# Kernel tuning notes

Measured on AMD Instinct MI355X. Metric: run time of the kernel, lower is better.

The kernel has to match this reference:

```python
import jax, jax.numpy as jnp
import numpy as np

NUM_HEADS = 8


def setup_inputs() -> dict:
    key = jax.random.key(0)
    k1, k2, k3, k4 = jax.random.split(key, 4)
    E = 256
    seq = jax.random.normal(k1, (4, 256, E, 16, 16), dtype=jnp.float32)
    W_qkv = jax.random.normal(k2, (3 * E, E), dtype=jnp.float32) * (E ** -0.5)
    W_out = jax.random.normal(k3, (E, E), dtype=jnp.float32) * (E ** -0.5)
    b_out = jax.random.normal(k4, (E,), dtype=jnp.float32)
    return {"seq": seq, "W_qkv": W_qkv, "W_out": W_out, "b_out": b_out,
            "n_sub_x": 16, "n_sub_y": 16}


def reference(seq, W_qkv, W_out, b_out, n_sub_x, n_sub_y):
    # seq: [b, s, c, h, w] -- a sequence of functions (tokens on spatial grids)
    b, s, c, h, w = seq.shape
    H = NUM_HEADS
    d = c // H  # head_dim

    # pointwise QKV projection along the channel axis (no bias)
    qkv = jnp.einsum('oc,bscxy->bsoxy', W_qkv, seq)  # [b, s, 3c, h, w]
    # channel layout per einops: (num_heads, split=3, head_dim)
    qkv = qkv.reshape(b, s, H, 3, d, h, w)
    qkv = jnp.transpose(qkv, (3, 0, 2, 1, 4, 5, 6))  # [3, b, H, s, d, h, w]
    q, k, v = qkv[0], qkv[1], qkv[2]

    # func_attention: L2 inner product over head_dim and spatial dims
    scale = 1.0 / np.sqrt(d * h * w).astype(np.float32)
    scores = jnp.einsum('bhqdxy,bhkdxy->bhqk', q, k) * scale  # [b, H, s, s]
    attn = jax.nn.softmax(scores, axis=-1)
    sa = jnp.einsum('bhqk,bhkdxy->bhqdxy', attn, v)  # [b, H, s, d, h, w]

    # merge heads back to channel axis: 'b h s d ... -> b s (h d) ...'
    sa = jnp.transpose(sa, (0, 2, 1, 3, 4, 5)).reshape(b, s, c, h, w)

    # output projection (with bias) along channels
    out = jnp.einsum('oc,bscxy->bsoxy', W_out, sa)
    out = out + b_out[None, None, :, None, None]
    return out
```

## Files before the change

kernel.cpp:

```cpp
#include <hip/hip_runtime.h>
#include <stdint.h>


#define DI __device__ __forceinline__

typedef __attribute__((ext_vector_type(4))) float  f32x4;
typedef __attribute__((ext_vector_type(8))) short  s16x8;
typedef __attribute__((ext_vector_type(4))) short  s16x4;
typedef __attribute__((ext_vector_type(8))) __bf16 bf16x8;

DI unsigned short f2bf(float f) {
    unsigned int u = __builtin_bit_cast(unsigned int, f);
    u = (u + 0x7fffu + ((u >> 16) & 1u)) >> 16;
    return (unsigned short)u;
}
DI bf16x8 asbf(s16x8 v) { return __builtin_bit_cast(bf16x8, v); }
#define MFMA16(a, b, c) __builtin_amdgcn_mfma_f32_16x16x32_bf16((a), (b), (c), 0, 0, 0)

DI void stage_a256(unsigned short* __restrict__ T,
                   const unsigned short* __restrict__ src, int stride, int tid) {
    const unsigned short* s = src + (size_t)tid * stride;
    int r7 = tid & 7;
#pragma unroll
    for (int ch = 0; ch < 8; ch++) {
        s16x8 v = *(const s16x8*)(s + ch * 8);
        *(s16x8*)&T[tid * 64 + ((ch ^ r7) << 3)] = v;
    }
}

DI void stage_l128(unsigned short* __restrict__ T,
                   const unsigned short* __restrict__ src, int stride, int tid) {
    int row = tid >> 1, c4 = (tid & 1) * 4, r7 = row & 7;
    const unsigned short* s = src + (size_t)row * stride;
#pragma unroll
    for (int i = 0; i < 4; i++) {
        s16x8 v = *(const s16x8*)(s + (c4 + i) * 8);
        *(s16x8*)&T[row * 64 + (((c4 + i) ^ r7) << 3)] = v;
    }
}

DI void stage_tr16(unsigned short* __restrict__ BT,
                   const unsigned short* __restrict__ src, int stride, int tid) {
    int p = tid & 127, cqh = tid >> 7, p7 = p & 7;
#pragma unroll
    for (int i = 0; i < 8; i++) {
        int cq = cqh + 2 * i;
        int cb = cq * 4;
        unsigned short e0 = src[(size_t)(cb + 0) * stride + p];
        unsigned short e1 = src[(size_t)(cb + 1) * stride + p];
        unsigned short e2 = src[(size_t)(cb + 2) * stride + p];
        unsigned short e3 = src[(size_t)(cb + 3) * stride + p];
        s16x4 v = {(short)e0, (short)e1, (short)e2, (short)e3};
        *(s16x4*)&BT[p * 64 + (((cq >> 1) ^ p7) << 3) + (cq & 1) * 4] = v;
    }
}

DI void stage_tr32(unsigned short* __restrict__ BT,
                   const float* __restrict__ src, int stride, int tid) {
    int p = tid & 127, cqh = tid >> 7, p7 = p & 7;
#pragma unroll
    for (int i = 0; i < 8; i++) {
        int cq = cqh + 2 * i;
        int cb = cq * 4;
        float e0 = src[(size_t)(cb + 0) * stride + p];
        float e1 = src[(size_t)(cb + 1) * stride + p];
        float e2 = src[(size_t)(cb + 2) * stride + p];
        float e3 = src[(size_t)(cb + 3) * stride + p];
        s16x4 v = {(short)f2bf(e0), (short)f2bf(e1), (short)f2bf(e2), (short)f2bf(e3)};
        *(s16x4*)&BT[p * 64 + (((cq >> 1) ^ p7) << 3) + (cq & 1) * 4] = v;
    }
}

DI void mfma_84(const unsigned short* __restrict__ Al,
                const unsigned short* __restrict__ Bl,
                f32x4 acc[8][4], int wm, int wn, int lg, int lr) {
#pragma unroll
    for (int kk = 0; kk < 2; kk++) {
        int off = (((kk * 4 + lg) ^ (lr & 7)) << 3);
        s16x8 af[8];
#pragma unroll
        for (int m = 0; m < 8; m++)
            af[m] = *(const s16x8*)&Al[(wm + m * 16 + lr) * 64 + off];
        s16x8 bf[4];
#pragma unroll
        for (int n = 0; n < 4; n++)
            bf[n] = *(const s16x8*)&Bl[(wn + n * 16 + lr) * 64 + off];
#pragma unroll
        for (int n = 0; n < 4; n++) {
            bf16x8 bv = asbf(bf[n]);
#pragma unroll
            for (int m = 0; m < 8; m++)
                acc[m][n] = MFMA16(asbf(af[m]), bv, acc[m][n]);
        }
    }
}

DI void mfma_44(const unsigned short* __restrict__ Al,
                const unsigned short* __restrict__ Bl,
                f32x4 acc[4][4], int wm, int wn, int lg, int lr) {
#pragma unroll
    for (int kk = 0; kk < 2; kk++) {
        int off = (((kk * 4 + lg) ^ (lr & 7)) << 3);
        s16x8 af[4];
#pragma unroll
        for (int m = 0; m < 4; m++)
            af[m] = *(const s16x8*)&Al[(wm + m * 16 + lr) * 64 + off];
        s16x8 bf[4];
#pragma unroll
        for (int n = 0; n < 4; n++)
            bf[n] = *(const s16x8*)&Bl[(wn + n * 16 + lr) * 64 + off];
#pragma unroll
        for (int n = 0; n < 4; n++) {
            bf16x8 bv = asbf(bf[n]);
#pragma unroll
            for (int m = 0; m < 4; m++)
                acc[m][n] = MFMA16(asbf(af[m]), bv, acc[m][n]);
        }
    }
}

__global__ __launch_bounds__(64) void k_prep(
    const float* __restrict__ Wqkv, const float* __restrict__ Wout,
    unsigned short* __restrict__ Wbf)
{
    int r = blockIdx.x, ln = threadIdx.x;
    const float* src;
    if (r < 768) {
        int split = r >> 8, hd = r & 255;
        src = Wqkv + (size_t)(((hd >> 5) * 96) + split * 32 + (hd & 31)) * 256;
    } else {
        src = Wout + (size_t)(r - 768) * 256;
    }
    f32x4 v = *(const f32x4*)(src + ln * 4);
    s16x4 h = {(short)f2bf(v.x), (short)f2bf(v.y), (short)f2bf(v.z), (short)f2bf(v.w)};
    *(s16x4*)&Wbf[(size_t)r * 256 + ln * 4] = h;
}

__global__ __launch_bounds__(256, 2) void k_qkv(
    const float* __restrict__ seq, const unsigned short* __restrict__ Wbf,
    unsigned short* __restrict__ Qb, unsigned short* __restrict__ Kb,
    unsigned short* __restrict__ Vb)
{
    const int bid = blockIdx.x;
    const int wk = (bid & 7) * 768 + (bid >> 3);
    const int bs = wk / 6, r6 = wk - bs * 6;
    const int mt = r6 >> 1, nt = r6 & 1;
    const int b = bs >> 8, s = bs & 255;
    const int tid = threadIdx.x, ln = tid & 63, wv = tid >> 6;
    const int wm = (wv >> 1) * 128, wn = (wv & 1) * 64;
    const int lg = ln >> 4, lr = ln & 15;

    __shared__ __align__(16) unsigned short Al[256 * 64];
    __shared__ __align__(16) unsigned short Bt[128 * 64];

    f32x4 acc[8][4];
    const f32x4 z4 = {0.f, 0.f, 0.f, 0.f};
#pragma unroll
    for (int m = 0; m < 8; m++)
#pragma unroll
        for (int n = 0; n < 4; n++) acc[m][n] = z4;

    const unsigned short* Asrc = Wbf + (size_t)mt * 256 * 256;
    const float* Bsrc = seq + (size_t)bs * 65536 + nt * 128;

    for (int k0 = 0; k0 < 256; k0 += 64) {
        stage_a256(Al, Asrc + k0, 256, tid);
        stage_tr32(Bt, Bsrc + (size_t)k0 * 256, 256, tid);
        __syncthreads();
        mfma_84(Al, Bt, acc, wm, wn, lg, lr);
        __syncthreads();
    }

    unsigned short* dst = (mt == 0) ? Qb : (mt == 1) ? Kb : Vb;
#pragma unroll
    for (int m = 0; m < 8; m++) {
#pragma unroll
        for (int rr = 0; rr < 4; rr++) {
            int o = wm + m * 16 + lg * 4 + rr;
            size_t base = ((size_t)((b * 8 + (o >> 5)) * 256 + s)) * 8192
                        + (size_t)(o & 31) * 256 + nt * 128 + wn + lr;
#pragma unroll
            for (int n = 0; n < 4; n++)
                dst[base + n * 16] = f2bf(acc[m][n][rr]);
        }
    }
}

__global__ __launch_bounds__(256, 3) void k_scores(
    const unsigned short* __restrict__ Qb, const unsigned short* __restrict__ Kb,
    float* __restrict__ Sp)
{
    const int bh = blockIdx.y;
    const int qt = blockIdx.x >> 2, kc = (blockIdx.x >> 1) & 1, st = blockIdx.x & 1;
    const int tid = threadIdx.x, ln = tid & 63, wv = tid >> 6;
    const int wm = (wv >> 1) * 64, wn = (wv & 1) * 64;
    const int lg = ln >> 4, lr = ln & 15;

    __shared__ __align__(16) unsigned short Al[128 * 64];
    __shared__ __align__(16) unsigned short Bl[128 * 64];

    f32x4 acc[4][4];
    const f32x4 z4 = {0.f, 0.f, 0.f, 0.f};
#pragma unroll
    for (int m = 0; m < 4; m++)
#pragma unroll
        for (int n = 0; n < 4; n++) acc[m][n] = z4;

    const unsigned short* Asrc = Qb + (size_t)(bh * 256 + qt * 128) * 8192 + kc * 4096;
    const unsigned short* Bsrc = Kb + (size_t)(bh * 256 + st * 128) * 8192 + kc * 4096;

    for (int t = 0; t < 64; t++) {
        stage_l128(Al, Asrc + t * 64, 8192, tid);
        stage_l128(Bl, Bsrc + t * 64, 8192, tid);
        __syncthreads();
        mfma_44(Al, Bl, acc, wm, wn, lg, lr);
        __syncthreads();
    }

    float* dst = Sp + (size_t)kc * 2097152
               + ((size_t)(bh * 256) + qt * 128 + wm) * 256 + st * 128 + wn;
#pragma unroll
    for (int m = 0; m < 4; m++) {
#pragma unroll
        for (int rr = 0; rr < 4; rr++) {
            float* d = dst + (size_t)(m * 16 + lg * 4 + rr) * 256 + lr;
#pragma unroll
            for (int n = 0; n < 4; n++)
                d[n * 16] = acc[m][n][rr];
        }
    }
}

__global__ __launch_bounds__(256) void k_softmax(
    const float* __restrict__ Sp, unsigned short* __restrict__ Pb)
{
    const int tid = threadIdx.x, ln = tid & 63;
    const int row = blockIdx.x * 4 + (tid >> 6);
    const float scale = 0.011048543456039806f;

    const float* p0 = Sp + (size_t)row * 256 + ln * 4;
    f32x4 a = *(const f32x4*)p0;
    f32x4 c = *(const f32x4*)(p0 + 2097152);
    f32x4 v = (a + c) * scale;

    float m = fmaxf(fmaxf(v.x, v.y), fmaxf(v.z, v.w));
#pragma unroll
    for (int off = 32; off; off >>= 1) m = fmaxf(m, __shfl_xor(m, off));
    float e0 = __expf(v.x - m), e1 = __expf(v.y - m);
    float e2 = __expf(v.z - m), e3 = __expf(v.w - m);
    float sum = e0 + e1 + e2 + e3;
#pragma unroll
    for (int off = 32; off; off >>= 1) sum += __shfl_xor(sum, off);
    float inv = 1.f / sum;
    s16x4 p = {(short)f2bf(e0 * inv), (short)f2bf(e1 * inv),
               (short)f2bf(e2 * inv), (short)f2bf(e3 * inv)};
    *(s16x4*)(Pb + (size_t)row * 256 + ln * 4) = p;
}

__global__ __launch_bounds__(256, 2) void k_av(
    const unsigned short* __restrict__ Pb, const unsigned short* __restrict__ Vb,
    unsigned short* __restrict__ SAb)
{
    const int ft = blockIdx.x, bh = blockIdx.y;
    const int b = bh >> 3, h = bh & 7;
    const int tid = threadIdx.x, ln = tid & 63, wv = tid >> 6;
    const int wm = (wv >> 1) * 128, wn = (wv & 1) * 64;
    const int lg = ln >> 4, lr = ln & 15;

    __shared__ __align__(16) unsigned short Al[256 * 64];
    __shared__ __align__(16) unsigned short Bt[128 * 64];

    f32x4 acc[8][4];
    const f32x4 z4 = {0.f, 0.f, 0.f, 0.f};
#pragma unroll
    for (int m = 0; m < 8; m++)
#pragma unroll
        for (int n = 0; n < 4; n++) acc[m][n] = z4;

    const unsigned short* Asrc = Pb + (size_t)(bh * 256) * 256;
    const unsigned short* Bsrc = Vb + (size_t)(bh * 256) * 8192 + ft * 128;

    for (int k0 = 0; k0 < 256; k0 += 64) {
        stage_a256(Al, Asrc + k0, 256, tid);
        stage_tr16(Bt, Bsrc + (size_t)k0 * 8192, 8192, tid);
        __syncthreads();
        mfma_84(Al, Bt, acc, wm, wn, lg, lr);
        __syncthreads();
    }

    const int cc = h * 32 + (ft >> 1);
    const int pb = (ft & 1) * 128;
#pragma unroll
    for (int m = 0; m < 8; m++) {
#pragma unroll
        for (int rr = 0; rr < 4; rr++) {
            int q = wm + m * 16 + lg * 4 + rr;
            size_t base = ((size_t)(b * 256 + q) * 256 + cc) * 256 + pb + wn + lr;
#pragma unroll
            for (int n = 0; n < 4; n++)
                SAb[base + n * 16] = f2bf(acc[m][n][rr]);
        }
    }
}

__global__ __launch_bounds__(256, 2) void k_out(
    const unsigned short* __restrict__ SAb, const unsigned short* __restrict__ Wbf,
    const float* __restrict__ bias, float* __restrict__ out)
{
    const int nt = blockIdx.x, bs = blockIdx.y;
    const int tid = threadIdx.x, ln = tid & 63, wv = tid >> 6;
    const int wm = (wv >> 1) * 128, wn = (wv & 1) * 64;
    const int lg = ln >> 4, lr = ln & 15;

    __shared__ __align__(16) unsigned short Al[256 * 64];
    __shared__ __align__(16) unsigned short Bt[128 * 64];

    f32x4 acc[8][4];
    const f32x4 z4 = {0.f, 0.f, 0.f, 0.f};
#pragma unroll
    for (int m = 0; m < 8; m++)
#pragma unroll
        for (int n = 0; n < 4; n++) acc[m][n] = z4;

    const unsigned short* Asrc = Wbf + (size_t)768 * 256;
    const unsigned short* Bsrc = SAb + (size_t)bs * 65536 + nt * 128;

    for (int k0 = 0; k0 < 256; k0 += 64) {
        stage_a256(Al, Asrc + k0, 256, tid);
        stage_tr16(Bt, Bsrc + (size_t)k0 * 256, 256, tid);
        __syncthreads();
        mfma_84(Al, Bt, acc, wm, wn, lg, lr);
        __syncthreads();
    }

#pragma unroll
    for (int m = 0; m < 8; m++) {
#pragma unroll
        for (int rr = 0; rr < 4; rr++) {
            int o = wm + m * 16 + lg * 4 + rr;
            float bo = bias[o];
            float* d = out + ((size_t)bs * 256 + o) * 256 + nt * 128 + wn + lr;
#pragma unroll
            for (int n = 0; n < 4; n++)
                d[n * 16] = acc[m][n][rr] + bo;
        }
    }
}

extern "C" void kernel_launch(void* const* d_in, const int* in_sizes, int n_in,
                              void* d_out, int out_size, void* d_ws, size_t ws_size,
                              hipStream_t stream)
{
    const float* seq  = (const float*)d_in[0];
    const float* Wqkv = (const float*)d_in[1];
    const float* Wout = (const float*)d_in[2];
    const float* bout = (const float*)d_in[3];

    unsigned short* Qb = (unsigned short*)d_out;
    unsigned short* Kb = Qb + 67108864;

    unsigned short* Vb  = (unsigned short*)d_ws;
    unsigned short* SAb = Vb + 67108864;
    float*          Sp  = (float*)SAb;
    unsigned short* Pb  = (unsigned short*)d_ws + 134217728;
    unsigned short* Wbf = Pb + 2097152;

    float* out = (float*)d_out;

    k_prep<<<dim3(1024), dim3(64), 0, stream>>>(Wqkv, Wout, Wbf);
    k_qkv<<<dim3(6144), dim3(256), 0, stream>>>(seq, Wbf, Qb, Kb, Vb);
    k_scores<<<dim3(8, 32), dim3(256), 0, stream>>>(Qb, Kb, Sp);
    k_softmax<<<dim3(2048), dim3(256), 0, stream>>>(Sp, Pb);
    k_av<<<dim3(64, 32), dim3(256), 0, stream>>>(Pb, Vb, SAb);
    k_out<<<dim3(2, 1024), dim3(256), 0, stream>>>(SAb, Wbf, bout, out);
}
```

Baseline: 604.8 us.

## Pre-transpose seq to bf16, split V projection with transposed layout, widen score split-K

```diff
diff --git a/kernel.cpp b/kernel.cpp
--- a/kernel.cpp
+++ b/kernel.cpp
@@ -39,34 +39,23 @@
     }
 }
 
-DI void stage_tr16(unsigned short* __restrict__ BT,
-                   const unsigned short* __restrict__ src, int stride, int tid) {
+DI void stage_tr16s(unsigned short* __restrict__ BT,
+                    const unsigned short* __restrict__ src, int stride, int tid) {
     int p = tid & 127, cqh = tid >> 7, p7 = p & 7;
+    unsigned short e[32];
+#pragma unroll
+    for (int i = 0; i < 8; i++) {
+        int cb = (cqh + 2 * i) * 4;
+        e[i * 4 + 0] = src[(size_t)(cb + 0) * stride + p];
+        e[i * 4 + 1] = src[(size_t)(cb + 1) * stride + p];
+        e[i * 4 + 2] = src[(size_t)(cb + 2) * stride + p];
+        e[i * 4 + 3] = src[(size_t)(cb + 3) * stride + p];
+    }
 #pragma unroll
     for (int i = 0; i < 8; i++) {
         int cq = cqh + 2 * i;
-        int cb = cq * 4;
-        unsigned short e0 = src[(size_t)(cb + 0) * stride + p];
-        unsigned short e1 = src[(size_t)(cb + 1) * stride + p];
-        unsigned short e2 = src[(size_t)(cb + 2) * stride + p];
-        unsigned short e3 = src[(size_t)(cb + 3) * stride + p];
-        s16x4 v = {(short)e0, (short)e1, (short)e2, (short)e3};
-        *(s16x4*)&BT[p * 64 + (((cq >> 1) ^ p7) << 3) + (cq & 1) * 4] = v;
-    }
-}
-
-DI void stage_tr32(unsigned short* __restrict__ BT,
-                   const float* __restrict__ src, int stride, int tid) {
-    int p = tid & 127, cqh = tid >> 7, p7 = p & 7;
-#pragma unroll
-    for (int i = 0; i < 8; i++) {
-        int cq = cqh + 2 * i;
-        int cb = cq * 4;
-        float e0 = src[(size_t)(cb + 0) * stride + p];
-        float e1 = src[(size_t)(cb + 1) * stride + p];
-        float e2 = src[(size_t)(cb + 2) * stride + p];
-        float e3 = src[(size_t)(cb + 3) * stride + p];
-        s16x4 v = {(short)f2bf(e0), (short)f2bf(e1), (short)f2bf(e2), (short)f2bf(e3)};
+        s16x4 v = {(short)e[i * 4 + 0], (short)e[i * 4 + 1],
+                   (short)e[i * 4 + 2], (short)e[i * 4 + 3]};
         *(s16x4*)&BT[p * 64 + (((cq >> 1) ^ p7) << 3) + (cq & 1) * 4] = v;
     }
 }
@@ -90,30 +79,6 @@
             bf16x8 bv = asbf(bf[n]);
 #pragma unroll
             for (int m = 0; m < 8; m++)
-                acc[m][n] = MFMA16(asbf(af[m]), bv, acc[m][n]);
-        }
-    }
-}
-
-DI void mfma_44(const unsigned short* __restrict__ Al,
-                const unsigned short* __restrict__ Bl,
-                f32x4 acc[4][4], int wm, int wn, int lg, int lr) {
-#pragma unroll
-    for (int kk = 0; kk < 2; kk++) {
-        int off = (((kk * 4 + lg) ^ (lr & 7)) << 3);
-        s16x8 af[4];
-#pragma unroll
-        for (int m = 0; m < 4; m++)
-            af[m] = *(const s16x8*)&Al[(wm + m * 16 + lr) * 64 + off];
-        s16x8 bf[4];
-#pragma unroll
-        for (int n = 0; n < 4; n++)
-            bf[n] = *(const s16x8*)&Bl[(wn + n * 16 + lr) * 64 + off];
-#pragma unroll
-        for (int n = 0; n < 4; n++) {
-            bf16x8 bv = asbf(bf[n]);
-#pragma unroll
-            for (int m = 0; m < 4; m++)
                 acc[m][n] = MFMA16(asbf(af[m]), bv, acc[m][n]);
         }
     }
@@ -136,15 +101,53 @@
     *(s16x4*)&Wbf[(size_t)r * 256 + ln * 4] = h;
 }
 
-__global__ __launch_bounds__(256, 2) void k_qkv(
-    const float* __restrict__ seq, const unsigned short* __restrict__ Wbf,
-    unsigned short* __restrict__ Qb, unsigned short* __restrict__ Kb,
-    unsigned short* __restrict__ Vb)
-{
-    const int bid = blockIdx.x;
-    const int wk = (bid & 7) * 768 + (bid >> 3);
-    const int bs = wk / 6, r6 = wk - bs * 6;
-    const int mt = r6 >> 1, nt = r6 & 1;
+__global__ __launch_bounds__(256) void k_tr(
+    const float* __restrict__ seq, unsigned short* __restrict__ seqT)
+{
+    const int bs = blockIdx.x, tid = threadIdx.x;
+    __shared__ __align__(16) unsigned short T[64][264];
+    const float* src = seq + (size_t)bs * 65536;
+    unsigned short* dst = seqT + (size_t)bs * 65536;
+
+    for (int co = 0; co < 256; co += 64) {
+        {
+            int r = tid >> 2, p0 = (tid & 3) * 64;
+            const float* s = src + (size_t)(co + r) * 256 + p0;
+#pragma unroll
+            for (int i = 0; i < 8; i++) {
+                f32x4 a = *(const f32x4*)(s + i * 8);
+                f32x4 b = *(const f32x4*)(s + i * 8 + 4);
+                s16x8 h = {(short)f2bf(a.x), (short)f2bf(a.y), (short)f2bf(a.z),
+                           (short)f2bf(a.w), (short)f2bf(b.x), (short)f2bf(b.y),
+                           (short)f2bf(b.z), (short)f2bf(b.w)};
+                *(s16x8*)&T[r][p0 + i * 8] = h;
+            }
+        }
+        __syncthreads();
+        {
+            unsigned short e[64];
+#pragma unroll
+            for (int c = 0; c < 64; c++) e[c] = T[c][tid];
+            unsigned short* d = dst + (size_t)tid * 256 + co;
+#pragma unroll
+            for (int j = 0; j < 8; j++) {
+                s16x8 v = {(short)e[j * 8 + 0], (short)e[j * 8 + 1],
+                           (short)e[j * 8 + 2], (short)e[j * 8 + 3],
+                           (short)e[j * 8 + 4], (short)e[j * 8 + 5],
+                           (short)e[j * 8 + 6], (short)e[j * 8 + 7]};
+                *(s16x8*)(d + j * 8) = v;
+            }
+        }
+        __syncthreads();
+    }
+}
+
+__global__ __launch_bounds__(256, 2) void k_qk(
+    const unsigned short* __restrict__ seqT, const unsigned short* __restrict__ Wbf,
+    unsigned short* __restrict__ Qb, unsigned short* __restrict__ Kb)
+{
+    const int x = blockIdx.x;
+    const int bs = x >> 2, mt = (x >> 1) & 1, nt = x & 1;
     const int b = bs >> 8, s = bs & 255;
     const int tid = threadIdx.x, ln = tid & 63, wv = tid >> 6;
     const int wm = (wv >> 1) * 128, wn = (wv & 1) * 64;
@@ -161,17 +164,17 @@
         for (int n = 0; n < 4; n++) acc[m][n] = z4;
 
     const unsigned short* Asrc = Wbf + (size_t)mt * 256 * 256;
-    const float* Bsrc = seq + (size_t)bs * 65536 + nt * 128;
+    const unsigned short* Bsrc = seqT + (size_t)bs * 65536 + (size_t)(nt * 128) * 256;
 
     for (int k0 = 0; k0 < 256; k0 += 64) {
         stage_a256(Al, Asrc + k0, 256, tid);
-        stage_tr32(Bt, Bsrc + (size_t)k0 * 256, 256, tid);
+        stage_l128(Bt, Bsrc + k0, 256, tid);
         __syncthreads();
         mfma_84(Al, Bt, acc, wm, wn, lg, lr);
         __syncthreads();
     }
 
-    unsigned short* dst = (mt == 0) ? Qb : (mt == 1) ? Kb : Vb;
+    unsigned short* dst = mt ? Kb : Qb;
 #pragma unroll
     for (int m = 0; m < 8; m++) {
 #pragma unroll
@@ -186,44 +189,89 @@
     }
 }
 
-__global__ __launch_bounds__(256, 3) void k_scores(
+__global__ __launch_bounds__(256, 2) void k_v(
+    const unsigned short* __restrict__ seqT, const unsigned short* __restrict__ Wbf,
+    unsigned short* __restrict__ Vt)
+{
+    const int x = blockIdx.x;
+    const int b = x >> 9, p = (x >> 1) & 255, nt = x & 1;
+    const int tid = threadIdx.x, ln = tid & 63, wv = tid >> 6;
+    const int wm = (wv >> 1) * 128, wn = (wv & 1) * 64;
+    const int lg = ln >> 4, lr = ln & 15;
+
+    __shared__ __align__(16) unsigned short Al[256 * 64];
+    __shared__ __align__(16) unsigned short Bt[128 * 64];
+
+    f32x4 acc[8][4];
+    const f32x4 z4 = {0.f, 0.f, 0.f, 0.f};
+#pragma unroll
+    for (int m = 0; m < 8; m++)
+#pragma unroll
+        for (int n = 0; n < 4; n++) acc[m][n] = z4;
+
+    const unsigned short* Asrc = Wbf + (size_t)512 * 256;
+    const unsigned short* Bsrc = seqT + ((size_t)(b * 256 + nt * 128)) * 65536
+                               + (size_t)p * 256;
+
+    for (int k0 = 0; k0 < 256; k0 += 64) {
+        stage_a256(Al, Asrc + k0, 256, tid);
+        stage_l128(Bt, Bsrc + k0, 65536, tid);
+        __syncthreads();
+        mfma_84(Al, Bt, acc, wm, wn, lg, lr);
+        __syncthreads();
+    }
+
+#pragma unroll
+    for (int m = 0; m < 8; m++) {
+#pragma unroll
+        for (int rr = 0; rr < 4; rr++) {
+            int o = wm + m * 16 + lg * 4 + rr;
+            size_t base = ((size_t)(b * 8 + (o >> 5)) * 8192
+                         + (size_t)(o & 31) * 256 + p) * 256 + nt * 128 + wn + lr;
+#pragma unroll
+            for (int n = 0; n < 4; n++)
+                Vt[base + n * 16] = f2bf(acc[m][n][rr]);
+        }
+    }
+}
+
+__global__ __launch_bounds__(256, 2) void k_scores(
     const unsigned short* __restrict__ Qb, const unsigned short* __restrict__ Kb,
     float* __restrict__ Sp)
 {
     const int bh = blockIdx.y;
-    const int qt = blockIdx.x >> 2, kc = (blockIdx.x >> 1) & 1, st = blockIdx.x & 1;
+    const int st = blockIdx.x >> 3, kc = blockIdx.x & 7;
     const int tid = threadIdx.x, ln = tid & 63, wv = tid >> 6;
-    const int wm = (wv >> 1) * 64, wn = (wv & 1) * 64;
+    const int wm = (wv >> 1) * 128, wn = (wv & 1) * 64;
     const int lg = ln >> 4, lr = ln & 15;
 
-    __shared__ __align__(16) unsigned short Al[128 * 64];
-    __shared__ __align__(16) unsigned short Bl[128 * 64];
-
-    f32x4 acc[4][4];
+    __shared__ __align__(16) unsigned short Al[256 * 64];
+    __shared__ __align__(16) unsigned short Bt[128 * 64];
+
+    f32x4 acc[8][4];
     const f32x4 z4 = {0.f, 0.f, 0.f, 0.f};
 #pragma unroll
-    for (int m = 0; m < 4; m++)
+    for (int m = 0; m < 8; m++)
 #pragma unroll
         for (int n = 0; n < 4; n++) acc[m][n] = z4;
 
-    const unsigned short* Asrc = Qb + (size_t)(bh * 256 + qt * 128) * 8192 + kc * 4096;
-    const unsigned short* Bsrc = Kb + (size_t)(bh * 256 + st * 128) * 8192 + kc * 4096;
-
-    for (int t = 0; t < 64; t++) {
-        stage_l128(Al, Asrc + t * 64, 8192, tid);
-        stage_l128(Bl, Bsrc + t * 64, 8192, tid);
-        __syncthreads();
-        mfma_44(Al, Bl, acc, wm, wn, lg, lr);
-        __syncthreads();
-    }
-
-    float* dst = Sp + (size_t)kc * 2097152
-               + ((size_t)(bh * 256) + qt * 128 + wm) * 256 + st * 128 + wn;
-#pragma unroll
-    for (int m = 0; m < 4; m++) {
+    const unsigned short* Asrc = Qb + (size_t)(bh * 256) * 8192 + kc * 1024;
+    const unsigned short* Bsrc = Kb + (size_t)(bh * 256 + st * 128) * 8192 + kc * 1024;
+
+    for (int t = 0; t < 16; t++) {
+        stage_a256(Al, Asrc + t * 64, 8192, tid);
+        stage_l128(Bt, Bsrc + t * 64, 8192, tid);
+        __syncthreads();
+        mfma_84(Al, Bt, acc, wm, wn, lg, lr);
+        __syncthreads();
+    }
+
+    float* dst = Sp + (size_t)kc * 2097152 + (size_t)(bh * 256) * 256 + st * 128;
+#pragma unroll
+    for (int m = 0; m < 8; m++) {
 #pragma unroll
         for (int rr = 0; rr < 4; rr++) {
-            float* d = dst + (size_t)(m * 16 + lg * 4 + rr) * 256 + lr;
+            float* d = dst + (size_t)(wm + m * 16 + lg * 4 + rr) * 256 + wn + lr;
 #pragma unroll
             for (int n = 0; n < 4; n++)
                 d[n * 16] = acc[m][n][rr];
@@ -239,9 +287,11 @@
     const float scale = 0.011048543456039806f;
 
     const float* p0 = Sp + (size_t)row * 256 + ln * 4;
-    f32x4 a = *(const f32x4*)p0;
-    f32x4 c = *(const f32x4*)(p0 + 2097152);
-    f32x4 v = (a + c) * scale;
+    f32x4 v = *(const f32x4*)p0;
+#pragma unroll
+    for (int k = 1; k < 8; k++)
+        v += *(const f32x4*)(p0 + (size_t)k * 2097152);
+    v *= scale;
 
     float m = fmaxf(fmaxf(v.x, v.y), fmaxf(v.z, v.w));
 #pragma unroll
@@ -258,7 +308,7 @@
 }
 
 __global__ __launch_bounds__(256, 2) void k_av(
-    const unsigned short* __restrict__ Pb, const unsigned short* __restrict__ Vb,
+    const unsigned short* __restrict__ Pb, const unsigned short* __restrict__ Vt,
     unsigned short* __restrict__ SAb)
 {
     const int ft = blockIdx.x, bh = blockIdx.y;
@@ -277,25 +327,24 @@
 #pragma unroll
         for (int n = 0; n < 4; n++) acc[m][n] = z4;
 
-    const unsigned short* Asrc = Pb + (size_t)(bh * 256) * 256;
-    const unsigned short* Bsrc = Vb + (size_t)(bh * 256) * 8192 + ft * 128;
+    const unsigned short* Asrc = Pb + (size_t)bh * 65536;
+    const unsigned short* Bsrc = Vt + (size_t)bh * 2097152 + (size_t)(ft * 128) * 256;
 
     for (int k0 = 0; k0 < 256; k0 += 64) {
         stage_a256(Al, Asrc + k0, 256, tid);
-        stage_tr16(Bt, Bsrc + (size_t)k0 * 8192, 8192, tid);
+        stage_l128(Bt, Bsrc + k0, 256, tid);
         __syncthreads();
         mfma_84(Al, Bt, acc, wm, wn, lg, lr);
         __syncthreads();
     }
 
-    const int cc = h * 32 + (ft >> 1);
-    const int pb = (ft & 1) * 128;
 #pragma unroll
     for (int m = 0; m < 8; m++) {
 #pragma unroll
         for (int rr = 0; rr < 4; rr++) {
             int q = wm + m * 16 + lg * 4 + rr;
-            size_t base = ((size_t)(b * 256 + q) * 256 + cc) * 256 + pb + wn + lr;
+            size_t base = (size_t)(b * 256 + q) * 65536 + h * 8192
+                        + ft * 128 + wn + lr;
 #pragma unroll
             for (int n = 0; n < 4; n++)
                 SAb[base + n * 16] = f2bf(acc[m][n][rr]);
@@ -327,7 +376,7 @@
 
     for (int k0 = 0; k0 < 256; k0 += 64) {
         stage_a256(Al, Asrc + k0, 256, tid);
-        stage_tr16(Bt, Bsrc + (size_t)k0 * 256, 256, tid);
+        stage_tr16s(Bt, Bsrc + (size_t)k0 * 256, 256, tid);
         __syncthreads();
         mfma_84(Al, Bt, acc, wm, wn, lg, lr);
         __syncthreads();
@@ -359,18 +408,21 @@
     unsigned short* Qb = (unsigned short*)d_out;
     unsigned short* Kb = Qb + 67108864;
 
-    unsigned short* Vb  = (unsigned short*)d_ws;
-    unsigned short* SAb = Vb + 67108864;
-    float*          Sp  = (float*)SAb;
-    unsigned short* Pb  = (unsigned short*)d_ws + 134217728;
-    unsigned short* Wbf = Pb + 2097152;
+    unsigned short* Vt   = (unsigned short*)d_ws;
+    unsigned short* seqT = Vt + 67108864;
+    float*          Sp   = (float*)seqT;
+    unsigned short* SAb  = seqT;
+    unsigned short* Pb   = (unsigned short*)d_ws + 134217728;
+    unsigned short* Wbf  = Pb + 2097152;
 
     float* out = (float*)d_out;
 
     k_prep<<<dim3(1024), dim3(64), 0, stream>>>(Wqkv, Wout, Wbf);
-    k_qkv<<<dim3(6144), dim3(256), 0, stream>>>(seq, Wbf, Qb, Kb, Vb);
-    k_scores<<<dim3(8, 32), dim3(256), 0, stream>>>(Qb, Kb, Sp);
+    k_tr<<<dim3(1024), dim3(256), 0, stream>>>(seq, seqT);
+    k_qk<<<dim3(4096), dim3(256), 0, stream>>>(seqT, Wbf, Qb, Kb);
+    k_v<<<dim3(2048), dim3(256), 0, stream>>>(seqT, Wbf, Vt);
+    k_scores<<<dim3(16, 32), dim3(256), 0, stream>>>(Qb, Kb, Sp);
     k_softmax<<<dim3(2048), dim3(256), 0, stream>>>(Sp, Pb);
-    k_av<<<dim3(64, 32), dim3(256), 0, stream>>>(Pb, Vb, SAb);
+    k_av<<<dim3(64, 32), dim3(256), 0, stream>>>(Pb, Vt, SAb);
     k_out<<<dim3(2, 1024), dim3(256), 0, stream>>>(SAb, Wbf, bout, out);
 }
```

After: 646.2 us. +6.9%, slower.
